# Performance work log

Measured on AMD Instinct MI355X. Metric: run time of the kernel, lower is better.

The kernel has to match this reference:

```python
import jax, jax.numpy as jnp
import numpy as np

D_EMB = 512
N_HEADS = 8
D_K = 64
D_V = 64
D_FF = 2048
N_LAYERS = 6
VOCAB = 32000
SRC_LEN = 512


def sin_enc_table(n_position, d):
    pos = jnp.arange(n_position, dtype=jnp.float32)[:, None]
    j = jnp.arange(d, dtype=jnp.float32)[None, :]
    angle = pos / jnp.power(10000.0, 2.0 * jnp.floor(j / 2.0) / d)
    return jnp.where((jnp.arange(d) % 2 == 0)[None, :], jnp.sin(angle), jnp.cos(angle))


def layer_norm(x, gamma, beta, eps=1e-5):
    mu = jnp.mean(x, axis=-1, keepdims=True)
    var = jnp.mean(jnp.square(x - mu), axis=-1, keepdims=True)
    return (x - mu) * jax.lax.rsqrt(var + eps) * gamma + beta


def setup_inputs() -> dict:
    key = jax.random.key(0)
    ks = jax.random.split(key, 20)
    s = 0.02
    L = N_LAYERS
    inp = {
        'enc_inputs': jax.random.randint(ks[0], (16, 512), 0, VOCAB),
        'emb': jax.random.normal(ks[1], (VOCAB, D_EMB), jnp.float32) * s,
        'Wq': jax.random.normal(ks[2], (L, N_HEADS * D_K, D_EMB), jnp.float32) * s,
        'bq': jnp.zeros((L, N_HEADS * D_K), jnp.float32),
        'Wk': jax.random.normal(ks[3], (L, N_HEADS * D_K, D_EMB), jnp.float32) * s,
        'bk': jnp.zeros((L, N_HEADS * D_K), jnp.float32),
        'Wv': jax.random.normal(ks[4], (L, N_HEADS * D_V, D_EMB), jnp.float32) * s,
        'bv': jnp.zeros((L, N_HEADS * D_V), jnp.float32),
        'Wo': jax.random.normal(ks[5], (L, D_EMB, N_HEADS * D_V), jnp.float32) * s,
        'bo': jnp.zeros((L, D_EMB), jnp.float32),
        'g1': jnp.ones((L, D_EMB), jnp.float32),
        'b1': jnp.zeros((L, D_EMB), jnp.float32),
        'Wc1': jax.random.normal(ks[6], (L, D_FF, D_EMB), jnp.float32) * s,
        'bc1': jnp.zeros((L, D_FF), jnp.float32),
        'Wc2': jax.random.normal(ks[7], (L, D_EMB, D_FF), jnp.float32) * s,
        'bc2': jnp.zeros((L, D_EMB), jnp.float32),
        'g2': jnp.ones((L, D_EMB), jnp.float32),
        'b2': jnp.zeros((L, D_EMB), jnp.float32),
    }
    return inp


def encoder_fwd(enc_inputs, emb, Wq, bq, Wk, bk, Wv, bv, Wo, bo, g1, b1, Wc1, bc1, Wc2, bc2, g2, b2):
    B, S = enc_inputs.shape
    pos_table = sin_enc_table(SRC_LEN + 1, D_EMB)  # frozen
    x = emb[enc_inputs] + pos_table[jnp.arange(1, S + 1)][None, :, :]
    # pad mask: True where key token == 0; broadcast over heads and queries
    pad = (enc_inputs == 0)[:, None, None, :]  # [B,1,1,S]
    scale = 1.0 / np.sqrt(D_K)
    attn_weights = []
    for l in range(N_LAYERS):
        residual = x
        q = (x @ Wq[l].T + bq[l]).reshape(B, S, N_HEADS, D_K).transpose(0, 2, 1, 3)
        k = (x @ Wk[l].T + bk[l]).reshape(B, S, N_HEADS, D_K).transpose(0, 2, 1, 3)
        v = (x @ Wv[l].T + bv[l]).reshape(B, S, N_HEADS, D_V).transpose(0, 2, 1, 3)
        scores = jnp.einsum('bhqd,bhkd->bhqk', q, k) * scale
        scores = jnp.where(pad, -1e9, scores)
        w = jax.nn.softmax(scores, axis=-1)
        ctx = jnp.einsum('bhqk,bhkd->bhqd', w, v)
        ctx = ctx.transpose(0, 2, 1, 3).reshape(B, S, N_HEADS * D_V)
        x = layer_norm(ctx @ Wo[l].T + bo[l] + residual, g1[l], b1[l])
        # position-wise FFN (conv1d k=1 == dense)
        h = jax.nn.relu(x @ Wc1[l].T + bc1[l])
        x = layer_norm(h @ Wc2[l].T + bc2[l] + x, g2[l], b2[l])
        attn_weights.append(w)
    return x, jnp.stack(attn_weights)


def reference(enc_inputs, emb, Wq, bq, Wk, bk, Wv, bv, Wo, bo, g1, b1, Wc1, bc1, Wc2, bc2, g2, b2):
    return encoder_fwd(enc_inputs, emb, Wq, bq, Wk, bk, Wv, bv, Wo, bo, g1, b1, Wc1, bc1, Wc2, bc2, g2, b2)
```

## Files before the change

kernel.cpp:

```cpp
#include <hip/hip_runtime.h>

typedef unsigned short u16;
typedef __attribute__((ext_vector_type(8))) short s16x8;
typedef __attribute__((ext_vector_type(4))) float f32x4;
typedef __attribute__((ext_vector_type(4))) unsigned short u16x4;

#define DEVI __device__ __forceinline__

DEVI float bf2f(u16 h) { union { unsigned u; float f; } v; v.u = ((unsigned)h) << 16; return v.f; }
DEVI u16 f2bf(float f) {
  union { unsigned u; float f; } v; v.f = f;
  unsigned u = v.u;
  unsigned r = (u + 0x7fffu + ((u >> 16) & 1u)) >> 16;
  return (u16)r;
}

DEVI f32x4 mfma16(s16x8 a, s16x8 b, f32x4 c) {
  return __builtin_amdgcn_mfma_f32_16x16x32_bf16(a, b, c, 0, 0, 0);
}

DEVI void cvt8(const float* __restrict__ in, u16* __restrict__ out, int i) {
  const f32x4* p = (const f32x4*)(in + (size_t)i * 8);
  f32x4 a = p[0], b = p[1];
  u16x4 o0 = { f2bf(a[0]), f2bf(a[1]), f2bf(a[2]), f2bf(a[3]) };
  u16x4 o1 = { f2bf(b[0]), f2bf(b[1]), f2bf(b[2]), f2bf(b[3]) };
  u16x4* q = (u16x4*)(out + (size_t)i * 8);
  q[0] = o0; q[1] = o1;
}

__global__ void prep_kern(const float* __restrict__ Wq, const float* __restrict__ Wk,
                          const float* __restrict__ Wv, const float* __restrict__ Wo,
                          const float* __restrict__ Wc1, const float* __restrict__ Wc2,
                          const float* __restrict__ bq, const float* __restrict__ bk,
                          const float* __restrict__ bv,
                          const int* __restrict__ tok, const float* __restrict__ emb,
                          u16* __restrict__ Wqkvb, u16* __restrict__ Wob,
                          u16* __restrict__ Wc1b, u16* __restrict__ Wc2b,
                          float* __restrict__ bqkvb, u16* __restrict__ xb) {
  const int Rqkv = 6 * 1536 * 512 / 8;
  const int Rwo  = 6 * 512 * 512 / 8;
  const int Rw1  = 6 * 2048 * 512 / 8;
  const int Rw2  = Rw1;
  const int Rb   = 6 * 1536 / 8;
  const int Remb = 8192 * 128;
  const int total = Rqkv + Rwo + Rw1 + Rw2 + Rb + Remb;
  for (int idx = blockIdx.x * blockDim.x + threadIdx.x; idx < total;
       idx += gridDim.x * blockDim.x) {
    int i = idx;
    if (i < Rqkv) {
      int c8 = i & 63;
      int t = i >> 6;
      int r = t % 1536, l = t / 1536;
      const float* src; int rr = r;
      if (r < 512) src = Wq;
      else if (r < 1024) { src = Wk; rr = r - 512; }
      else { src = Wv; rr = r - 1024; }
      const f32x4* p = (const f32x4*)(src + ((size_t)(l * 512 + rr) * 512) + c8 * 8);
      f32x4 a = p[0], b = p[1];
      u16x4 o0 = { f2bf(a[0]), f2bf(a[1]), f2bf(a[2]), f2bf(a[3]) };
      u16x4 o1 = { f2bf(b[0]), f2bf(b[1]), f2bf(b[2]), f2bf(b[3]) };
      u16x4* q = (u16x4*)(Wqkvb + (size_t)i * 8);
      q[0] = o0; q[1] = o1;
      continue;
    }
    i -= Rqkv;
    if (i < Rwo) { cvt8(Wo, Wob, i); continue; }
    i -= Rwo;
    if (i < Rw1) { cvt8(Wc1, Wc1b, i); continue; }
    i -= Rw1;
    if (i < Rw2) { cvt8(Wc2, Wc2b, i); continue; }
    i -= Rw2;
    if (i < Rb) {
      #pragma unroll
      for (int u = 0; u < 8; ++u) {
        int j = i * 8 + u;
        int l = j / 1536, r = j % 1536;
        float v = (r < 512) ? bq[l * 512 + r]
                : (r < 1024) ? bk[l * 512 + r - 512] : bv[l * 512 + r - 1024];
        bqkvb[j] = v;
      }
      continue;
    }
    i -= Rb;
    {
      int bs = i >> 7;
      int t = i & 127;
      int s = bs & 511;
      int id = tok[bs];
      float pos = (float)(s + 1);
      int j0 = t * 4;
      f32x4 e = *(const f32x4*)(emb + (size_t)id * 512 + j0);
      u16x4 ob;
      #pragma unroll
      for (int u = 0; u < 4; ++u) {
        int j = j0 + u;
        float expo = (float)(j & ~1) * (1.0f / 512.0f);
        float ang = pos / powf(10000.0f, expo);
        float pe = (j & 1) ? cosf(ang) : sinf(ang);
        ob[u] = f2bf(e[u] + pe);
      }
      *(u16x4*)(xb + (size_t)bs * 512 + j0) = ob;
    }
  }
}

template <int WM, bool RELU, bool VT>
__global__ __launch_bounds__(256, 2) void gemm_bs(const u16* __restrict__ A,
                                                  const u16* __restrict__ Bt,
                                                  const float* __restrict__ bias,
                                                  u16* __restrict__ Cb, u16* __restrict__ Vt,
                                                  int N, int K, int nN) {
  constexpr int MF = WM / 16;
  constexpr int RPB = WM * 4;
  __shared__ __align__(16) u16 Bsw[128 * 256];

  const int chunkw = gridDim.x >> 3;
  const int wgid = (blockIdx.x & 7) * chunkw + (blockIdx.x >> 3);
  const int n = wgid % nN, m = wgid / nN;
  const int bn0 = n * 128, bm0 = m * RPB;

  const int tid = threadIdx.x, lane = tid & 63, wid = tid >> 6;
  const int l15 = lane & 15, lhi = lane >> 4;
  const int mrow0 = bm0 + wid * WM;

  f32x4 acc[MF][8];
  #pragma unroll
  for (int i = 0; i < MF; ++i)
    #pragma unroll
    for (int j = 0; j < 8; ++j)
      #pragma unroll
      for (int r = 0; r < 4; ++r) acc[i][j][r] = 0.0f;

  const u16* aB[MF];
  #pragma unroll
  for (int i = 0; i < MF; ++i)
    aB[i] = A + (size_t)(mrow0 + i * 16 + l15) * K + lhi * 8;

  const int rounds = K >> 8;
  for (int r = 0; r < rounds; ++r) {
    const int kb = r << 8;
    s16x8 tmp[16];
    #pragma unroll
    for (int c = 0; c < 16; ++c) {
      int cc = c * 256 + tid;
      int row = cc >> 5, col = cc & 31;
      tmp[c] = *(const s16x8*)(Bt + (size_t)(bn0 + row) * K + kb + col * 8);
    }
    __syncthreads();
    #pragma unroll
    for (int c = 0; c < 16; ++c) {
      int cc = c * 256 + tid;
      int row = cc >> 5, col = cc & 31;
      int byte = row * 512 + ((col * 16) ^ ((row & 7) << 4));
      *(s16x8*)((char*)Bsw + byte) = tmp[c];
    }
    __syncthreads();
    #pragma unroll
    for (int ks = 0; ks < 8; ++ks) {
      s16x8 af[MF], bf[8];
      #pragma unroll
      for (int i = 0; i < MF; ++i)
        af[i] = *(const s16x8*)(aB[i] + kb + ks * 32);
      #pragma unroll
      for (int j = 0; j < 8; ++j) {
        int row = j * 16 + l15;
        int byte = row * 512 + (((ks * 64) + lhi * 16) ^ ((row & 7) << 4));
        bf[j] = *(const s16x8*)((char*)Bsw + byte);
      }
      #pragma unroll
      for (int i = 0; i < MF; ++i)
        #pragma unroll
        for (int j = 0; j < 8; ++j)
          acc[i][j] = mfma16(af[i], bf[j], acc[i][j]);
    }
  }

  const int r0 = mrow0 + lhi * 4;
  const int c0 = bn0 + l15;
  if (VT && bn0 >= 1024) {
    __syncthreads();
    u16* T = Bsw;
    #pragma unroll
    for (int i = 0; i < MF; ++i)
      #pragma unroll
      for (int j = 0; j < 8; ++j) {
        int col = c0 + j * 16;
        float bv = bias[col];
        int lr0 = wid * WM + i * 16 + lhi * 4;
        int lc = j * 16 + l15;
        #pragma unroll
        for (int r = 0; r < 4; ++r)
          T[(lr0 + r) * 136 + lc] = f2bf(acc[i][j][r] + bv);
      }
    __syncthreads();
    const int b = bm0 >> 9, s0 = bm0 & 511;
    for (int c = tid; c < 2048; c += 256) {
      int dr = c >> 4;
      int ch = c & 15;
      s16x8 v;
      #pragma unroll
      for (int k = 0; k < 8; ++k) v[k] = T[(ch * 8 + k) * 136 + dr];
      int hc = bn0 - 1024 + dr;
      int h = hc >> 6, d = hc & 63;
      *(s16x8*)&Vt[((size_t)((b * 8 + h) * 64 + d)) * 512 + s0 + ch * 8] = v;
    }
  } else {
    #pragma unroll
    for (int i = 0; i < MF; ++i)
      #pragma unroll
      for (int j = 0; j < 8; ++j) {
        int col = c0 + j * 16;
        float bv = bias[col];
        #pragma unroll
        for (int r = 0; r < 4; ++r) {
          int row = r0 + i * 16 + r;
          float v = acc[i][j][r] + bv;
          if (RELU) v = fmaxf(v, 0.0f);
          Cb[(size_t)row * N + col] = f2bf(v);
        }
      }
  }
}

__global__ void ln2_kern(const u16* __restrict__ parts,
                         const u16* __restrict__ resid,
                         const float* __restrict__ gam, const float* __restrict__ bet,
                         float* __restrict__ outf, u16* __restrict__ outb) {
  int row = blockIdx.x * 4 + (threadIdx.x >> 6);
  int t = threadIdx.x & 63;
  size_t base = (size_t)row * 512;
  const u16x4* pp = (const u16x4*)(parts + base);
  u16x4 pa = pp[t], pb4 = pp[t + 64];
  const u16x4* rp = (const u16x4*)(resid + base);
  u16x4 ra = rp[t], rb = rp[t + 64];
  f32x4 v0, v1;
  #pragma unroll
  for (int u = 0; u < 4; ++u) {
    v0[u] = bf2f(pa[u]) + bf2f(ra[u]);
    v1[u] = bf2f(pb4[u]) + bf2f(rb[u]);
  }

  float s = v0[0] + v0[1] + v0[2] + v0[3] + v1[0] + v1[1] + v1[2] + v1[3];
  float q = v0[0]*v0[0] + v0[1]*v0[1] + v0[2]*v0[2] + v0[3]*v0[3]
          + v1[0]*v1[0] + v1[1]*v1[1] + v1[2]*v1[2] + v1[3]*v1[3];
  #pragma unroll
  for (int d = 1; d < 64; d <<= 1) { s += __shfl_xor(s, d, 64); q += __shfl_xor(q, d, 64); }
  float mu = s * (1.0f / 512.0f);
  float var = q * (1.0f / 512.0f) - mu * mu;
  float rs = rsqrtf(var + 1e-5f);
  const f32x4* gp = (const f32x4*)gam;
  const f32x4* bp = (const f32x4*)bet;
  f32x4 ga = gp[t], gb = gp[t + 64], ba = bp[t], bb = bp[t + 64];
  f32x4 o0, o1; u16x4 ob0, ob1;
  #pragma unroll
  for (int u = 0; u < 4; ++u) {
    float a0 = (v0[u] - mu) * rs * ga[u] + ba[u];
    float a1 = (v1[u] - mu) * rs * gb[u] + bb[u];
    o0[u] = a0; o1[u] = a1; ob0[u] = f2bf(a0); ob1[u] = f2bf(a1);
  }
  u16x4* obp = (u16x4*)(outb + base);
  obp[t] = ob0; obp[t + 64] = ob1;
  if (outf) {
    f32x4* op = (f32x4*)(outf + base);
    op[t] = o0; op[t + 64] = o1;
  }
}

__global__ void attn_kern(const u16* __restrict__ QKV, const u16* __restrict__ Vt,
                          const int* __restrict__ tok,
                          float* __restrict__ wout, u16* __restrict__ ctxb) {
  int wg = (blockIdx.x & 7) * 256 + (blockIdx.x >> 3);
  int qt = wg & 15;
  int h = (wg >> 4) & 7;
  int b = wg >> 7;
  int tid = threadIdx.x;
  int lane = tid & 63, wid = tid >> 6;
  int l15 = lane & 15, lhi = lane >> 4;
  int m0 = qt * 32;

  __shared__ __align__(16) u16 Wl[32][528];
  __shared__ float pmask[512];
  __shared__ float redbuf[2][32][4];

  for (int c = tid; c < 512; c += 256)
    pmask[c] = (tok[b * 512 + c] == 0) ? 1.0f : 0.0f;

  s16x8 qf[2][2];
  const u16* qbase = QKV + (size_t)(b * 512 + m0) * 1536 + h * 64;
  #pragma unroll
  for (int i = 0; i < 2; ++i)
    #pragma unroll
    for (int kk = 0; kk < 2; ++kk)
      qf[i][kk] = *(const s16x8*)(qbase + (size_t)(i * 16 + l15) * 1536 + kk * 32 + lhi * 8);

  f32x4 sacc[2][8];
  #pragma unroll
  for (int i = 0; i < 2; ++i)
    #pragma unroll
    for (int j = 0; j < 8; ++j)
      #pragma unroll
      for (int r = 0; r < 4; ++r) sacc[i][j][r] = 0.0f;

  int c0 = wid * 128;
  const u16* kbase = QKV + (size_t)(b * 512 + c0) * 1536 + 512 + h * 64;
  #pragma unroll
  for (int j = 0; j < 8; ++j) {
    #pragma unroll
    for (int kk = 0; kk < 2; ++kk) {
      s16x8 kf = *(const s16x8*)(kbase + (size_t)(j * 16 + l15) * 1536 + kk * 32 + lhi * 8);
      sacc[0][j] = mfma16(qf[0][kk], kf, sacc[0][j]);
      sacc[1][j] = mfma16(qf[1][kk], kf, sacc[1][j]);
    }
  }
  __syncthreads();

  float rm[2][4], sm[2][4], gi[2][4];
  #pragma unroll
  for (int i = 0; i < 2; ++i)
    #pragma unroll
    for (int r = 0; r < 4; ++r) rm[i][r] = -3.0e38f;

  #pragma unroll
  for (int j = 0; j < 8; ++j) {
    float pm = pmask[c0 + j * 16 + l15];
    #pragma unroll
    for (int i = 0; i < 2; ++i)
      #pragma unroll
      for (int r = 0; r < 4; ++r) {
        float sv = sacc[i][j][r] * 0.125f;
        sv = (pm != 0.0f) ? -1.0e9f : sv;
        sacc[i][j][r] = sv;
        rm[i][r] = fmaxf(rm[i][r], sv);
      }
  }
  #pragma unroll
  for (int d = 1; d < 16; d <<= 1)
    #pragma unroll
    for (int i = 0; i < 2; ++i)
      #pragma unroll
      for (int r = 0; r < 4; ++r)
        rm[i][r] = fmaxf(rm[i][r], __shfl_xor(rm[i][r], d, 64));

  if (l15 == 0) {
    #pragma unroll
    for (int i = 0; i < 2; ++i)
      #pragma unroll
      for (int r = 0; r < 4; ++r)
        redbuf[0][i * 16 + lhi * 4 + r][wid] = rm[i][r];
  }
  __syncthreads();
  #pragma unroll
  for (int i = 0; i < 2; ++i)
    #pragma unroll
    for (int r = 0; r < 4; ++r) {
      int row = i * 16 + lhi * 4 + r;
      rm[i][r] = fmaxf(fmaxf(redbuf[0][row][0], redbuf[0][row][1]),
                       fmaxf(redbuf[0][row][2], redbuf[0][row][3]));
      sm[i][r] = 0.0f;
    }
  #pragma unroll
  for (int j = 0; j < 8; ++j)
    #pragma unroll
    for (int i = 0; i < 2; ++i)
      #pragma unroll
      for (int r = 0; r < 4; ++r) {
        float pv = __expf(sacc[i][j][r] - rm[i][r]);
        sacc[i][j][r] = pv;
        sm[i][r] += pv;
      }
  #pragma unroll
  for (int d = 1; d < 16; d <<= 1)
    #pragma unroll
    for (int i = 0; i < 2; ++i)
      #pragma unroll
      for (int r = 0; r < 4; ++r)
        sm[i][r] += __shfl_xor(sm[i][r], d, 64);
  if (l15 == 0) {
    #pragma unroll
    for (int i = 0; i < 2; ++i)
      #pragma unroll
      for (int r = 0; r < 4; ++r)
        redbuf[1][i * 16 + lhi * 4 + r][wid] = sm[i][r];
  }
  __syncthreads();
  #pragma unroll
  for (int i = 0; i < 2; ++i)
    #pragma unroll
    for (int r = 0; r < 4; ++r) {
      int row = i * 16 + lhi * 4 + r;
      float tot = redbuf[1][row][0] + redbuf[1][row][1] + redbuf[1][row][2] + redbuf[1][row][3];
      gi[i][r] = 1.0f / tot;
    }

  float* wrow = wout + ((size_t)((b * 8 + h) * 512 + m0)) * 512;
  #pragma unroll
  for (int j = 0; j < 8; ++j)
    #pragma unroll
    for (int i = 0; i < 2; ++i)
      #pragma unroll
      for (int r = 0; r < 4; ++r) {
        float wv = sacc[i][j][r] * gi[i][r];
        int row = i * 16 + lhi * 4 + r;
        int col = c0 + j * 16 + l15;
        Wl[row][col] = f2bf(wv);
        wrow[(size_t)row * 512 + col] = wv;
      }
  __syncthreads();

  f32x4 cacc[2];
  #pragma unroll
  for (int i = 0; i < 2; ++i)
    #pragma unroll
    for (int r = 0; r < 4; ++r) cacc[i][r] = 0.0f;
  const u16* vbase = Vt + ((size_t)((b * 8 + h) * 64 + wid * 16 + l15)) * 512;
  #pragma unroll
  for (int kk = 0; kk < 16; ++kk) {
    s16x8 vf = *(const s16x8*)(vbase + kk * 32 + lhi * 8);
    #pragma unroll
    for (int i = 0; i < 2; ++i) {
      s16x8 wf = *(const s16x8*)&Wl[i * 16 + l15][kk * 32 + lhi * 8];
      cacc[i] = mfma16(wf, vf, cacc[i]);
    }
  }

  __syncthreads();
  u16* ct = &Wl[0][0];
  #pragma unroll
  for (int i = 0; i < 2; ++i)
    #pragma unroll
    for (int r = 0; r < 4; ++r)
      ct[(i * 16 + lhi * 4 + r) * 72 + wid * 16 + l15] = f2bf(cacc[i][r]);
  __syncthreads();
  {
    int row = tid >> 3, col = (tid & 7) * 8;
    s16x8 v = *(const s16x8*)&ct[row * 72 + col];
    *(s16x8*)&ctxb[(size_t)(b * 512 + m0 + row) * 512 + h * 64 + col] = v;
  }
}

extern "C" void kernel_launch(void* const* d_in, const int* in_sizes, int n_in,
                              void* d_out, int out_size, void* d_ws, size_t ws_size,
                              hipStream_t stream) {
  const int*   tok = (const int*)d_in[0];
  const float* emb = (const float*)d_in[1];
  const float* Wq  = (const float*)d_in[2];
  const float* bq  = (const float*)d_in[3];
  const float* Wk  = (const float*)d_in[4];
  const float* bk  = (const float*)d_in[5];
  const float* Wv  = (const float*)d_in[6];
  const float* bv  = (const float*)d_in[7];
  const float* Wo  = (const float*)d_in[8];
  const float* bo  = (const float*)d_in[9];
  const float* g1  = (const float*)d_in[10];
  const float* b1  = (const float*)d_in[11];
  const float* Wc1 = (const float*)d_in[12];
  const float* bc1 = (const float*)d_in[13];
  const float* Wc2 = (const float*)d_in[14];
  const float* bc2 = (const float*)d_in[15];
  const float* g2  = (const float*)d_in[16];
  const float* b2  = (const float*)d_in[17];
  (void)in_sizes; (void)n_in; (void)out_size; (void)ws_size;

  float* out_x = (float*)d_out;
  float* out_w = out_x + (size_t)16 * 512 * 512;

  char* p = (char*)d_ws;
  size_t off = 0;
  auto alloc = [&](size_t bytes) { char* r = p + off; off += (bytes + 255) & ~(size_t)255; return r; };
  u16*   xb  = (u16*)alloc((size_t)8192 * 512 * 2);
  u16*   pwo = (u16*)alloc((size_t)8192 * 512 * 2);
  char*  regA = alloc((size_t)8192 * 1536 * 2 + (size_t)8192 * 512 * 2);
  u16* QKVb = (u16*)regA;
  u16* Vtb  = QKVb + (size_t)8192 * 1536;
  u16* hb   = (u16*)regA;
  u16* ctxb = (u16*)alloc((size_t)8192 * 512 * 2);
  u16* Wqkvb = (u16*)alloc((size_t)6 * 1536 * 512 * 2);
  u16* Wob   = (u16*)alloc((size_t)6 * 512 * 512 * 2);
  u16* Wc1b  = (u16*)alloc((size_t)6 * 2048 * 512 * 2);
  u16* Wc2b  = (u16*)alloc((size_t)6 * 2048 * 512 * 2);
  float* bqkvb = (float*)alloc((size_t)6 * 1536 * 4);

  prep_kern<<<2048, 256, 0, stream>>>(Wq, Wk, Wv, Wo, Wc1, Wc2, bq, bk, bv, tok, emb,
                                      Wqkvb, Wob, Wc1b, Wc2b, bqkvb, xb);

  for (int l = 0; l < 6; ++l) {
    const u16* wqkv_l = Wqkvb + (size_t)l * 1536 * 512;
    const u16* wo_l = Wob + (size_t)l * 512 * 512;
    const u16* w1_l = Wc1b + (size_t)l * 2048 * 512;
    const u16* w2_l = Wc2b + (size_t)l * 2048 * 512;

    gemm_bs<32, false, true><<<768, 256, 0, stream>>>(xb, wqkv_l, bqkvb + l * 1536,
                                                      QKVb, Vtb, 1536, 512, 12);
    attn_kern<<<2048, 256, 0, stream>>>(QKVb, Vtb, tok,
                                        out_w + (size_t)l * 8 * 16 * 512 * 512, ctxb);
    gemm_bs<16, false, false><<<512, 256, 0, stream>>>(ctxb, wo_l, bo + l * 512,
                                                       pwo, nullptr, 512, 512, 4);
    ln2_kern<<<2048, 256, 0, stream>>>(pwo, xb, g1 + l * 512, b1 + l * 512, nullptr, xb);
    gemm_bs<32, true, false><<<1024, 256, 0, stream>>>(xb, w1_l, bc1 + l * 2048,
                                                       hb, nullptr, 2048, 512, 16);
    gemm_bs<16, false, false><<<512, 256, 0, stream>>>(hb, w2_l, bc2 + l * 512,
                                                       pwo, nullptr, 512, 2048, 4);
    ln2_kern<<<2048, 256, 0, stream>>>(pwo, xb, g2 + l * 512, b2 + l * 512,
                                       (l == 5 ? out_x : nullptr), xb);
  }
}
```

Measured before the change: 1.036 ms.

## Stage K/V tiles in swizzled LDS and coalesce attention-weight stores

The attention kernel now copies each wave's K slice and V^T slice from global memory into a per-wave XOR-swizzled LDS buffer, and the MFMA operands are read from LDS instead of through strided global loads. The fp32 attention weights, previously written as scattered scalar stores, are staged in LDS and written out as coalesced 16-byte vector stores. Launch bounds of 256 threads with one block per SM are added. Shared memory rises by 64 KB per block, which limits occupancy and adds extra LDS traffic and barriers.

Result: slower. 1.197 ms (+15.5%).

```diff
diff --git a/kernel.cpp b/kernel.cpp
--- a/kernel.cpp
+++ b/kernel.cpp
@@ -266,9 +266,11 @@
   }
 }
 
-__global__ void attn_kern(const u16* __restrict__ QKV, const u16* __restrict__ Vt,
-                          const int* __restrict__ tok,
-                          float* __restrict__ wout, u16* __restrict__ ctxb) {
+__global__ __launch_bounds__(256, 1) void attn_kern(const u16* __restrict__ QKV,
+                                                    const u16* __restrict__ Vt,
+                                                    const int* __restrict__ tok,
+                                                    float* __restrict__ wout,
+                                                    u16* __restrict__ ctxb) {
   int wg = (blockIdx.x & 7) * 256 + (blockIdx.x >> 3);
   int qt = wg & 15;
   int h = (wg >> 4) & 7;
@@ -278,10 +280,14 @@
   int l15 = lane & 15, lhi = lane >> 4;
   int m0 = qt * 32;
 
+  __shared__ __align__(16) char KV[4][16384];
   __shared__ __align__(16) u16 Wl[32][528];
   __shared__ float pmask[512];
   __shared__ float redbuf[2][32][4];
 
+  char* myKV = KV[wid];
+  int c0 = wid * 128;
+
   for (int c = tid; c < 512; c += 256)
     pmask[c] = (tok[b * 512 + c] == 0) ? 1.0f : 0.0f;
 
@@ -293,6 +299,19 @@
     for (int kk = 0; kk < 2; ++kk)
       qf[i][kk] = *(const s16x8*)(qbase + (size_t)(i * 16 + l15) * 1536 + kk * 32 + lhi * 8);
 
+  {
+    const u16* kg = QKV + (size_t)(b * 512 + c0) * 1536 + 512 + h * 64;
+    #pragma unroll
+    for (int it = 0; it < 16; ++it) {
+      int ch = it * 64 + lane;
+      int row = ch >> 3, d0 = (ch & 7) * 8;
+      s16x8 v = *(const s16x8*)(kg + (size_t)row * 1536 + d0);
+      int byte = row * 128 + ((d0 * 2) ^ ((row & 7) << 4));
+      *(s16x8*)(myKV + byte) = v;
+    }
+  }
+  __syncthreads();
+
   f32x4 sacc[2][8];
   #pragma unroll
   for (int i = 0; i < 2; ++i)
@@ -301,18 +320,27 @@
       #pragma unroll
       for (int r = 0; r < 4; ++r) sacc[i][j][r] = 0.0f;
 
-  int c0 = wid * 128;
-  const u16* kbase = QKV + (size_t)(b * 512 + c0) * 1536 + 512 + h * 64;
-  #pragma unroll
-  for (int j = 0; j < 8; ++j) {
+  #pragma unroll
+  for (int j = 0; j < 8; ++j)
     #pragma unroll
     for (int kk = 0; kk < 2; ++kk) {
-      s16x8 kf = *(const s16x8*)(kbase + (size_t)(j * 16 + l15) * 1536 + kk * 32 + lhi * 8);
+      int row = j * 16 + l15;
+      int byte = row * 128 + ((kk * 64 + lhi * 16) ^ ((row & 7) << 4));
+      s16x8 kf = *(const s16x8*)(myKV + byte);
       sacc[0][j] = mfma16(qf[0][kk], kf, sacc[0][j]);
       sacc[1][j] = mfma16(qf[1][kk], kf, sacc[1][j]);
     }
-  }
-  __syncthreads();
+
+  {
+    const u16* vg = Vt + ((size_t)((b * 8 + h) * 64 + wid * 16)) * 512;
+    #pragma unroll
+    for (int it = 0; it < 16; ++it) {
+      int s0 = lane * 8;
+      s16x8 v = *(const s16x8*)(vg + (size_t)it * 512 + s0);
+      int byte = it * 1024 + ((s0 * 2) ^ ((it & 7) << 4));
+      *(s16x8*)(myKV + byte) = v;
+    }
+  }
 
   float rm[2][4], sm[2][4], gi[2][4];
   #pragma unroll
@@ -392,7 +420,6 @@
       gi[i][r] = 1.0f / tot;
     }
 
-  float* wrow = wout + ((size_t)((b * 8 + h) * 512 + m0)) * 512;
   #pragma unroll
   for (int j = 0; j < 8; ++j)
     #pragma unroll
@@ -400,10 +427,8 @@
       #pragma unroll
       for (int r = 0; r < 4; ++r) {
         float wv = sacc[i][j][r] * gi[i][r];
-        int row = i * 16 + lhi * 4 + r;
-        int col = c0 + j * 16 + l15;
-        Wl[row][col] = f2bf(wv);
-        wrow[(size_t)row * 512 + col] = wv;
+        sacc[i][j][r] = wv;
+        Wl[i * 16 + lhi * 4 + r][c0 + j * 16 + l15] = f2bf(wv);
       }
   __syncthreads();
 
@@ -412,29 +437,47 @@
   for (int i = 0; i < 2; ++i)
     #pragma unroll
     for (int r = 0; r < 4; ++r) cacc[i][r] = 0.0f;
-  const u16* vbase = Vt + ((size_t)((b * 8 + h) * 64 + wid * 16 + l15)) * 512;
   #pragma unroll
   for (int kk = 0; kk < 16; ++kk) {
-    s16x8 vf = *(const s16x8*)(vbase + kk * 32 + lhi * 8);
+    int byte = l15 * 1024 + ((kk * 64 + lhi * 16) ^ ((l15 & 7) << 4));
+    s16x8 vf = *(const s16x8*)(myKV + byte);
     #pragma unroll
     for (int i = 0; i < 2; ++i) {
       s16x8 wf = *(const s16x8*)&Wl[i * 16 + l15][kk * 32 + lhi * 8];
       cacc[i] = mfma16(wf, vf, cacc[i]);
     }
   }
-
   __syncthreads();
+
   u16* ct = &Wl[0][0];
   #pragma unroll
   for (int i = 0; i < 2; ++i)
     #pragma unroll
     for (int r = 0; r < 4; ++r)
       ct[(i * 16 + lhi * 4 + r) * 72 + wid * 16 + l15] = f2bf(cacc[i][r]);
+  float* wq = (float*)myKV;
+  #pragma unroll
+  for (int j = 0; j < 8; ++j)
+    #pragma unroll
+    for (int i = 0; i < 2; ++i)
+      #pragma unroll
+      for (int r = 0; r < 4; ++r)
+        wq[(i * 16 + lhi * 4 + r) * 128 + j * 16 + l15] = sacc[i][j][r];
   __syncthreads();
+
   {
     int row = tid >> 3, col = (tid & 7) * 8;
     s16x8 v = *(const s16x8*)&ct[row * 72 + col];
     *(s16x8*)&ctxb[(size_t)(b * 512 + m0 + row) * 512 + h * 64 + col] = v;
+  }
+  float* wrow = wout + ((size_t)((b * 8 + h) * 512 + m0)) * 512;
+  #pragma unroll
+  for (int it = 0; it < 16; ++it) {
+    int c = it * 256 + tid;
+    int grow = c >> 7;
+    int cc = c & 127;
+    const f32x4* src = (const f32x4*)(KV[cc >> 5] + grow * 512 + (cc & 31) * 16);
+    *(f32x4*)(wrow + (size_t)grow * 512 + cc * 4) = *src;
   }
 }
 
```
